# Kernel optimization log

Hardware: AMD Instinct MI355X
Metric: run time of the kernel (lower is better)

Reference implementation:

```python
import jax, jax.numpy as jnp
import numpy as np

B, T, C, NH = 2, 2048, 1024, 16
HD = C // NH  # 64


def _ln(x, g, b, eps=1e-5):
    m = x.mean(-1, keepdims=True)
    v = ((x - m) ** 2).mean(-1, keepdims=True)
    return (x - m) / jnp.sqrt(v + eps) * g + b


def _ff(x, w1, b1, w2, b2):
    # Linear -> exact (erf) GELU -> Linear; dropout=0 (identity)
    return jax.nn.gelu(x @ w1 + b1, approximate=False) @ w2 + b2


def setup_inputs() -> dict:
    key = jax.random.key(0)
    ks = jax.random.split(key, 16)
    s = 0.02
    f32 = jnp.float32
    return {
        "x": jax.random.normal(ks[0], (B, T, C), f32),
        # SelfAttn qkv projection (torch Linear stored transposed: (in, out))
        "w_attn": jax.random.normal(ks[1], (C, 3 * C), f32) * s,
        "b_attn": jnp.zeros((3 * C,), f32),
        # SelfAttn's internal FeedForward
        "wa1": jax.random.normal(ks[2], (C, 4 * C), f32) * s,
        "ba1": jnp.zeros((4 * C,), f32),
        "wa2": jax.random.normal(ks[3], (4 * C, C), f32) * s,
        "ba2": jnp.zeros((C,), f32),
        # Block ln1
        "g1": jnp.ones((C,), f32),
        "be1": jnp.zeros((C,), f32),
        # Block FeedForward
        "wf1": jax.random.normal(ks[4], (C, 4 * C), f32) * s,
        "bf1": jnp.zeros((4 * C,), f32),
        "wf2": jax.random.normal(ks[5], (4 * C, C), f32) * s,
        "bf2": jnp.zeros((C,), f32),
        # Block ln2
        "g2": jnp.ones((C,), f32),
        "be2": jnp.zeros((C,), f32),
    }


def reference(x, w_attn, b_attn, wa1, ba1, wa2, ba2, g1, be1,
              wf1, bf1, wf2, bf2, g2, be2):
    Bx, Tx, Cx = x.shape
    qkv = x @ w_attn + b_attn  # (B, T, 3C)
    # NOTE: original splits as K, Q, V (in that order)
    K, Q, V = jnp.split(qkv, 3, axis=-1)

    def heads(t):  # (B, T, C) -> (B, NH, T, HD)
        return t.reshape(Bx, Tx, NH, HD).transpose(0, 2, 1, 3)

    Q, K, V = heads(Q), heads(K), heads(V)
    att = jnp.einsum('bhqd,bhkd->bhqk', Q, K) / np.float32(np.sqrt(HD))
    mask = jnp.tril(jnp.ones((Tx, Tx), bool))  # causal
    att = jnp.where(mask, att, -jnp.inf)
    att = jax.nn.softmax(att, axis=-1)
    y = jnp.einsum('bhqk,bhkd->bhqd', att, V)
    y = y.transpose(0, 2, 1, 3).reshape(Bx, Tx, Cx)
    # SelfAttn applies its own FeedForward (no output projection)
    y = _ff(y, wa1, ba1, wa2, ba2)
    # Block: post-sublayer LayerNorm, additive residuals
    x = x + _ln(y, g1, be1)
    x = x + _ln(_ff(x, wf1, bf1, wf2, bf2), g2, be2)
    return x
```

## Files before the change

kernel.cpp:

```cpp
#include <hip/hip_runtime.h>
#include <hip/hip_bf16.h>
#include <math.h>

#define Bz 2
#define Tz 2048
#define Cz 1024
#define NHz 16
#define HDz 64
#define Mz (Bz*Tz)

typedef unsigned short u16;
typedef __attribute__((ext_vector_type(8))) short bf16x8;
typedef __attribute__((ext_vector_type(4))) float f32x4;

__device__ __forceinline__ float bf2f(u16 u){
  union { unsigned int i; float f; } v; v.i = ((unsigned int)u) << 16; return v.f;
}
__device__ __forceinline__ u16 f2bf(float f){
  union { float f; unsigned int i; } v; v.f = f;
  return (u16)((v.i + 0x7fffu + ((v.i >> 16) & 1u)) >> 16);
}
__device__ __forceinline__ unsigned pack_bf_trunc(float a, float b){
  union { float f; unsigned u; } ua, ub; ua.f = a; ub.f = b;
  return (ua.u >> 16) | (ub.u & 0xffff0000u);
}
__device__ __forceinline__ float gelu_fast(float x){
  float x3 = x * x * x;
  float z2 = 1.5957691216057308f * (x + 0.044715f * x3);
  float e  = __expf(z2);
  float t  = 1.f - 2.f / (e + 1.f);
  return 0.5f * x * (1.f + t);
}

__device__ __forceinline__ void glds16(const void* g, void* l){
  __builtin_amdgcn_global_load_lds(
      (const __attribute__((address_space(1))) void*)g,
      (__attribute__((address_space(3))) void*)l, 16, 0, 0);
}

__device__ __forceinline__ void pbar(){
  asm volatile("" ::: "memory");
  __builtin_amdgcn_s_barrier();
  asm volatile("" ::: "memory");
}
#define VMCNT(n) asm volatile("s_waitcnt vmcnt(" #n ")" ::: "memory")

__global__ __launch_bounds__(256) void cast4_kernel(const float* __restrict__ in,
                                                    u16* __restrict__ out, int n4){
  int i = blockIdx.x * 256 + threadIdx.x;
  if (i < n4) {
    float4 v = ((const float4*)in)[i];
    u16 t[4] = { f2bf(v.x), f2bf(v.y), f2bf(v.z), f2bf(v.w) };
    *(uint2*)&out[(size_t)i * 4] = *(const uint2*)t;
  }
}

__global__ __launch_bounds__(256) void transpose5_kernel(
    const float* __restrict__ s0, const float* __restrict__ s1,
    const float* __restrict__ s2, const float* __restrict__ s3,
    const float* __restrict__ s4,
    u16* __restrict__ d0, u16* __restrict__ d1, u16* __restrict__ d2,
    u16* __restrict__ d3, u16* __restrict__ d4){
  __shared__ float tile[32][33];
  const int t = blockIdx.x;
  const float* src; u16* dst; int K, N, local;
  if (t < 3072)       { src = s0; dst = d0; K = 1024; N = 3072; local = t; }
  else if (t < 7168)  { src = s1; dst = d1; K = 1024; N = 4096; local = t - 3072; }
  else if (t < 11264) { src = s2; dst = d2; K = 4096; N = 1024; local = t - 7168; }
  else if (t < 15360) { src = s3; dst = d3; K = 1024; N = 4096; local = t - 11264; }
  else                { src = s4; dst = d4; K = 4096; N = 1024; local = t - 15360; }
  const int NT = N >> 5;
  const int kb = (local / NT) * 32, nb = (local % NT) * 32;
  const int tx = threadIdx.x & 31, ty = threadIdx.x >> 5;
  #pragma unroll
  for (int r = ty; r < 32; r += 8)
    tile[r][tx] = src[(size_t)(kb + r) * N + nb + tx];
  __syncthreads();
  #pragma unroll
  for (int r = ty; r < 32; r += 8)
    dst[(size_t)(nb + r) * K + kb + tx] = f2bf(tile[tx][r]);
}

template<int ACT>
__global__ __launch_bounds__(512, 2) void gemm256_kernel(const u16* __restrict__ A,
                                                         const u16* __restrict__ Bt,
                                                         const float* __restrict__ bias,
                                                         u16* __restrict__ ob,
                                                         int N, int lda, int klen){
  __shared__ __align__(16) u16 As[2][256 * 64];
  __shared__ __align__(16) u16 Bs[2][256 * 64];
  const int tid  = threadIdx.x;
  const int lane = tid & 63;
  const int wave = tid >> 6;
  const int cc = lane & 15, quad = lane >> 4;
  const int wm = (wave >> 2) * 128;
  const int wn = (wave & 3) * 64;

  int flat = blockIdx.x + gridDim.x * blockIdx.y;
  const int nwg = gridDim.x * gridDim.y;
  flat = (flat & 7) * (nwg >> 3) + (flat >> 3);
  const int m0 = (flat & 15) * 256;
  const int n0 = (flat >> 4) * 256;

  const u16* Ak  = A  + (size_t)blockIdx.z * klen;
  const u16* Btk = Bt + (size_t)blockIdx.z * klen;

  int srow[2], scol[2];
  #pragma unroll
  for (int rnd = 0; rnd < 2; ++rnd) {
    const int ci = tid + rnd * 512;
    const int r = ci >> 3, cg = ci & 7;
    srow[rnd] = r;
    scol[rnd] = (cg ^ (r & 7)) * 8;
  }
  int colsw[2];
  #pragma unroll
  for (int s = 0; s < 2; ++s)
    colsw[s] = (s * 32 + quad * 8) ^ ((cc & 7) << 3);

  const auto stA = [&](int h, int t) {
    u16* dst = &As[t & 1][h * 8192];
    const u16* src = Ak + (size_t)(m0 + h * 128) * lda + t * 64;
    #pragma unroll
    for (int rnd = 0; rnd < 2; ++rnd)
      glds16(src + (size_t)srow[rnd] * lda + scol[rnd], dst + (tid + rnd * 512) * 8);
  };
  const auto stB = [&](int h, int t) {
    u16* dst = &Bs[t & 1][h * 8192];
    const u16* src = Btk + (size_t)(n0 + h * 128) * lda + t * 64;
    #pragma unroll
    for (int rnd = 0; rnd < 2; ++rnd)
      glds16(src + (size_t)srow[rnd] * lda + scol[rnd], dst + (tid + rnd * 512) * 8);
  };

  bf16x8 af[4][2];
  bf16x8 bfr[2][2][2];
  f32x4 acc[2][2][4][2] = {};

  const auto rdA = [&](int qa, int bsel) {
    #pragma unroll
    for (int f = 0; f < 4; ++f)
      #pragma unroll
      for (int s = 0; s < 2; ++s)
        af[f][s] = *(const bf16x8*)&As[bsel][(wm + qa * 64 + f * 16 + cc) * 64 + colsw[s]];
  };
  const auto rdB = [&](int qb, int bsel) {
    #pragma unroll
    for (int f = 0; f < 2; ++f)
      #pragma unroll
      for (int s = 0; s < 2; ++s)
        bfr[qb][f][s] = *(const bf16x8*)&Bs[bsel][(wn + qb * 32 + f * 16 + cc) * 64 + colsw[s]];
  };
  const auto mf16 = [&](int qa, int qb) {
    __builtin_amdgcn_s_setprio(1);
    #pragma unroll
    for (int s = 0; s < 2; ++s)
      #pragma unroll
      for (int am = 0; am < 4; ++am)
        #pragma unroll
        for (int bn = 0; bn < 2; ++bn)
          acc[qa][qb][am][bn] = __builtin_amdgcn_mfma_f32_16x16x32_bf16(
              af[am][s], bfr[qb][bn][s], acc[qa][qb][am][bn], 0, 0, 0);
    __builtin_amdgcn_s_setprio(0);
  };

  stA(0, 0); stB(0, 0); stA(1, 0); stB(1, 0);
  stA(0, 1); stB(1, 1);
  VMCNT(4);
  pbar();

  const int nIter = klen >> 7;
  for (int i = 0; i < nIter; ++i) {
    const int t = 2 * i;
    const bool more = (i + 1 < nIter);
    rdA(0, 0); rdB(0, 0); stA(1, t + 1);
    pbar(); mf16(0, 0); pbar();
    rdB(1, 0); stB(0, t + 1);
    pbar(); mf16(0, 1); pbar();
    rdA(1, 0); if (more) stA(0, t + 2);
    pbar(); mf16(1, 1); pbar();
    if (more) stB(1, t + 2);
    pbar(); mf16(1, 0);
    if (more) { VMCNT(4); } else { VMCNT(0); }
    pbar();
    rdA(0, 1); rdB(0, 1); if (more) stA(1, t + 2);
    pbar(); mf16(0, 0); pbar();
    rdB(1, 1); if (more) stB(0, t + 2);
    pbar(); mf16(0, 1); pbar();
    rdA(1, 1); if (more) stA(0, t + 3);
    pbar(); mf16(1, 1); pbar();
    if (more) stB(1, t + 3);
    pbar(); mf16(1, 0);
    if (more) { VMCNT(4); }
    pbar();
  }

  u16* obz = ob + (size_t)blockIdx.z * ((size_t)Mz * N);
  const float* bp = (blockIdx.z == 0) ? bias : nullptr;
  #pragma unroll
  for (int qa = 0; qa < 2; ++qa)
    #pragma unroll
    for (int qb = 0; qb < 2; ++qb)
      #pragma unroll
      for (int bn = 0; bn < 2; ++bn) {
        const int col = n0 + wn + qb * 32 + bn * 16 + cc;
        const float bv = bp ? bp[col] : 0.f;
        #pragma unroll
        for (int am = 0; am < 4; ++am)
          #pragma unroll
          for (int r = 0; r < 4; ++r) {
            const int row = m0 + wm + qa * 64 + am * 16 + quad * 4 + r;
            float v = acc[qa][qb][am][bn][r] + bv;
            if (ACT == 1) v = gelu_fast(v);
            obz[(size_t)row * N + col] = f2bf(v);
          }
      }
}

__global__ __launch_bounds__(256) void vtrans_kernel(const u16* __restrict__ qkv,
                                                     u16* __restrict__ Vtb){
  __shared__ u16 Vl[64 * 72];
  const int tid = threadIdx.x;
  const int t0 = blockIdx.x * 64, h = blockIdx.y, b = blockIdx.z;
  const int bh = b * NHz + h;
  #pragma unroll
  for (int it = 0; it < 2; it++) {
    int c = tid + it * 256;
    int row = c >> 3, g = c & 7;
    *(uint4*)&Vl[row * 72 + g * 8] =
        *(const uint4*)(qkv + (size_t)(b * Tz + t0 + row) * (3 * Cz) + 2 * Cz + h * 64 + g * 8);
  }
  __syncthreads();
  #pragma unroll
  for (int it = 0; it < 2; it++) {
    int c = tid + it * 256;
    int d = c >> 3, tg = c & 7;
    u16 tmp[8];
    #pragma unroll
    for (int e = 0; e < 8; e++) tmp[e] = Vl[(tg * 8 + e) * 72 + d];
    *(uint4*)&Vtb[((size_t)bh * 64 + d) * Tz + t0 + tg * 8] = *(const uint4*)tmp;
  }
}

__global__ __launch_bounds__(256) void attn_kernel(const u16* __restrict__ qkv,
                                                   const u16* __restrict__ Vtb,
                                                   u16* __restrict__ y){
  __shared__ __align__(16) u16 KV[2][2][64 * 64];
  __shared__ __align__(16) u16 Ps[64 * 72];
  const int tid = threadIdx.x;
  const int lane = tid & 63, wave = tid >> 6;
  const int cc = lane & 15, quad = lane >> 4;
  const int h = blockIdx.y, b = blockIdx.z;
  const int bh = b * NHz + h;
  const size_t rowb = (size_t)b * Tz;
  const int wq0 = wave * 16;

  int foff[4][2];
  const int sw0 = (quad ^ (cc & 7)) * 8;
  const int sw1 = ((4 + quad) ^ (cc & 7)) * 8;
  #pragma unroll
  for (int t = 0; t < 4; ++t) {
    foff[t][0] = (t * 16 + cc) * 64 + sw0;
    foff[t][1] = (t * 16 + cc) * 64 + sw1;
  }
  const int pswb = (wq0 + cc) * 72 + quad * 4;
  const int psr0 = (wq0 + cc) * 72 + quad * 8;
  const int psr1 = (wq0 + cc) * 72 + 32 + quad * 8;

  auto stage = [&](int i, int bsel) {
    const int k0s = i * 64;
    #pragma unroll
    for (int it = 0; it < 2; ++it) {
      int ci = tid + it * 256;
      int row = ci >> 3, g = ci & 7;
      int gs = g ^ (row & 7);
      glds16(qkv + (rowb + k0s + row) * (3 * Cz) + h * 64 + gs * 8, &KV[bsel][0][ci * 8]);
      glds16(Vtb + ((size_t)bh * 64 + row) * Tz + k0s + gs * 8,     &KV[bsel][1][ci * 8]);
    }
  };

  for (int ph = 0; ph < 2; ++ph) {
    const int qt = ph ? (31 - (int)blockIdx.x) : (int)blockIdx.x;
    const int q0t = qt * 64 + wq0;
    const int nkt = qt + 1;
    const int wqmax = q0t + 15;

    bf16x8 qf[2];
    #pragma unroll
    for (int s = 0; s < 2; ++s)
      qf[s] = *(const bf16x8*)(qkv + (rowb + q0t + cc) * (3 * Cz)
                               + Cz + h * 64 + s * 32 + quad * 8);
    f32x4 acc[4] = {};
    float lp = 0.f;

    if (ph) __syncthreads();
    stage(0, 0);

    for (int i = 0; i < nkt; ++i) {
      __syncthreads();
      if (i + 1 < nkt) stage(i + 1, (i + 1) & 1);
      const int sel = i & 1;
      const u16* Kl = KV[sel][0];
      const u16* Vl = KV[sel][1];
      const int k0 = i * 64;
      if (k0 > wqmax) continue;

      bf16x8 kf[4][2];
      #pragma unroll
      for (int kt = 0; kt < 4; ++kt) {
        kf[kt][0] = *(const bf16x8*)&Kl[foff[kt][0]];
        kf[kt][1] = *(const bf16x8*)&Kl[foff[kt][1]];
      }
      const int qbase = q0t;
      #pragma unroll
      for (int kt = 0; kt < 4; ++kt) {
        const int kbase = k0 + kt * 16;
        uint2 pk;
        if (kbase > qbase + 15) {
          pk.x = 0u; pk.y = 0u;
        } else {
          f32x4 st = __builtin_amdgcn_mfma_f32_16x16x32_bf16(
              kf[kt][0], qf[0], (f32x4){0.f, 0.f, 0.f, 0.f}, 0, 0, 0);
          st = __builtin_amdgcn_mfma_f32_16x16x32_bf16(kf[kt][1], qf[1], st, 0, 0, 0);
          if (kbase + 15 > qbase) {
            const int kq = kbase + quad * 4, ql = qbase + cc;
            st[0] = (kq     <= ql) ? st[0] : -1e30f;
            st[1] = (kq + 1 <= ql) ? st[1] : -1e30f;
            st[2] = (kq + 2 <= ql) ? st[2] : -1e30f;
            st[3] = (kq + 3 <= ql) ? st[3] : -1e30f;
          }
          float p0 = __expf(fmaf(st[0], 0.125f, -16.f));
          float p1 = __expf(fmaf(st[1], 0.125f, -16.f));
          float p2 = __expf(fmaf(st[2], 0.125f, -16.f));
          float p3 = __expf(fmaf(st[3], 0.125f, -16.f));
          lp += (p0 + p1) + (p2 + p3);
          pk.x = pack_bf_trunc(p0, p1);
          pk.y = pack_bf_trunc(p2, p3);
        }
        *(uint2*)&Ps[pswb + kt * 16] = pk;
      }
      bf16x8 pf0 = *(const bf16x8*)&Ps[psr0];
      bf16x8 pf1 = *(const bf16x8*)&Ps[psr1];
      #pragma unroll
      for (int jd = 0; jd < 4; ++jd) {
        bf16x8 vf0 = *(const bf16x8*)&Vl[foff[jd][0]];
        bf16x8 vf1 = *(const bf16x8*)&Vl[foff[jd][1]];
        acc[jd] = __builtin_amdgcn_mfma_f32_16x16x32_bf16(pf0, vf0, acc[jd], 0, 0, 0);
        acc[jd] = __builtin_amdgcn_mfma_f32_16x16x32_bf16(pf1, vf1, acc[jd], 0, 0, 0);
      }
    }

    lp += __shfl_xor(lp, 16, 64);
    lp += __shfl_xor(lp, 32, 64);
    float inv[4];
    #pragma unroll
    for (int r = 0; r < 4; ++r) inv[r] = 1.f / __shfl(lp, quad * 4 + r, 64);
    #pragma unroll
    for (int jd = 0; jd < 4; ++jd)
      #pragma unroll
      for (int r = 0; r < 4; ++r) {
        int qrow = q0t + quad * 4 + r;
        y[(rowb + qrow) * Cz + h * 64 + jd * 16 + cc] = f2bf(acc[jd][r] * inv[r]);
      }
  }
}

__global__ __launch_bounds__(256) void ln_resid_kernel(const float* __restrict__ xf,
                                                       const u16* __restrict__ xb16,
                                                       const u16* __restrict__ yp,
                                                       const float* __restrict__ g,
                                                       const float* __restrict__ be,
                                                       float* __restrict__ outf,
                                                       u16* __restrict__ outb){
  const int row = blockIdx.x;
  const int c0 = threadIdx.x * 4;
  const size_t base = (size_t)row * Cz + c0;
  float4 v; v.x = 0.f; v.y = 0.f; v.z = 0.f; v.w = 0.f;
  #pragma unroll
  for (int p = 0; p < 4; ++p) {
    uint2 pp = *(const uint2*)(yp + (size_t)p * ((size_t)Mz * Cz) + base);
    v.x += bf2f((u16)(pp.x & 0xffff)); v.y += bf2f((u16)(pp.x >> 16));
    v.z += bf2f((u16)(pp.y & 0xffff)); v.w += bf2f((u16)(pp.y >> 16));
  }
  float s  = v.x + v.y + v.z + v.w;
  float s2 = v.x*v.x + v.y*v.y + v.z*v.z + v.w*v.w;
  #pragma unroll
  for (int off = 32; off > 0; off >>= 1) {
    s  += __shfl_down(s,  off);
    s2 += __shfl_down(s2, off);
  }
  __shared__ float ps[4], ps2[4];
  int wave = threadIdx.x >> 6, lane = threadIdx.x & 63;
  if (lane == 0) { ps[wave] = s; ps2[wave] = s2; }
  __syncthreads();
  s  = ps[0]  + ps[1]  + ps[2]  + ps[3];
  s2 = ps2[0] + ps2[1] + ps2[2] + ps2[3];
  const float mean = s * (1.f / Cz);
  const float var  = s2 * (1.f / Cz) - mean * mean;
  const float rstd = rsqrtf(var + 1e-5f);
  float4 xv;
  if (xf) {
    xv = *(const float4*)(xf + base);
  } else {
    uint2 px = *(const uint2*)(xb16 + base);
    xv.x = bf2f((u16)(px.x & 0xffff)); xv.y = bf2f((u16)(px.x >> 16));
    xv.z = bf2f((u16)(px.y & 0xffff)); xv.w = bf2f((u16)(px.y >> 16));
  }
  float4 gv = *(const float4*)(g + c0);
  float4 bv = *(const float4*)(be + c0);
  float4 ov;
  ov.x = xv.x + (v.x - mean) * rstd * gv.x + bv.x;
  ov.y = xv.y + (v.y - mean) * rstd * gv.y + bv.y;
  ov.z = xv.z + (v.z - mean) * rstd * gv.z + bv.z;
  ov.w = xv.w + (v.w - mean) * rstd * gv.w + bv.w;
  if (outf) *(float4*)(outf + base) = ov;
  if (outb) {
    u16 t[4] = { f2bf(ov.x), f2bf(ov.y), f2bf(ov.z), f2bf(ov.w) };
    *(ulonglong1*)&outb[base] = *(const ulonglong1*)t;
  }
}

extern "C" void kernel_launch(void* const* d_in, const int* in_sizes, int n_in,
                              void* d_out, int out_size, void* d_ws, size_t ws_size,
                              hipStream_t stream) {
  const float* x      = (const float*)d_in[0];
  const float* w_attn = (const float*)d_in[1];
  const float* b_attn = (const float*)d_in[2];
  const float* wa1    = (const float*)d_in[3];
  const float* ba1    = (const float*)d_in[4];
  const float* wa2    = (const float*)d_in[5];
  const float* ba2    = (const float*)d_in[6];
  const float* g1     = (const float*)d_in[7];
  const float* be1    = (const float*)d_in[8];
  const float* wf1    = (const float*)d_in[9];
  const float* bf1    = (const float*)d_in[10];
  const float* wf2    = (const float*)d_in[11];
  const float* bf2    = (const float*)d_in[12];
  const float* g2     = (const float*)d_in[13];
  const float* be2    = (const float*)d_in[14];
  float* out = (float*)d_out;

  char* ws = (char*)d_ws;
  size_t off = 0;
  auto alloc = [&](size_t bytes) { size_t o = off; off += (bytes + 255) & ~(size_t)255; return o; };
  u16* qkvb    = (u16*)(ws + alloc((size_t)Mz * 3 * Cz * 2));
  u16* ybuf    = (u16*)(ws + alloc((size_t)Mz * Cz * 2));
  u16* xb      = (u16*)(ws + alloc((size_t)Mz * Cz * 2));
  u16* wT_attn = (u16*)(ws + alloc((size_t)3 * Cz * Cz * 2));
  u16* wT_a1   = (u16*)(ws + alloc((size_t)4 * Cz * Cz * 2));
  u16* Vtb     = (u16*)(ws + alloc((size_t)Bz * NHz * HDz * Tz * 2));
  u16* wT_a2   = (u16*)(ws + alloc((size_t)4 * Cz * Cz * 2));
  u16* wT_f1   = (u16*)(ws + alloc((size_t)4 * Cz * Cz * 2));
  u16* wT_f2   = (u16*)(ws + alloc((size_t)4 * Cz * Cz * 2));
  u16* hbuf    = (u16*)(ws + alloc((size_t)Mz * 4 * Cz * 2));
  u16* pb      = (u16*)(ws + alloc((size_t)4 * Mz * Cz * 2));
  u16* x1b     = (u16*)(ws + alloc((size_t)Mz * Cz * 2));
  alloc(256);
  (void)ws_size; (void)in_sizes; (void)n_in; (void)out_size;

  cast4_kernel<<<(Mz * Cz / 4 + 255) / 256, 256, 0, stream>>>(x, xb, Mz * Cz / 4);
  transpose5_kernel<<<19456, 256, 0, stream>>>(w_attn, wa1, wa2, wf1, wf2,
                                               wT_attn, wT_a1, wT_a2, wT_f1, wT_f2);

  gemm256_kernel<0><<<dim3(16, 12, 1), 512, 0, stream>>>(xb, wT_attn, b_attn,
      qkvb, 3*Cz, Cz, Cz);

  vtrans_kernel<<<dim3(Tz/64, NHz, Bz), 256, 0, stream>>>(qkvb, Vtb);
  attn_kernel<<<dim3(16, NHz, Bz), 256, 0, stream>>>(qkvb, Vtb, ybuf);

  gemm256_kernel<1><<<dim3(16, 16, 1), 512, 0, stream>>>(ybuf, wT_a1, ba1,
      hbuf, 4*Cz, Cz, Cz);
  gemm256_kernel<0><<<dim3(16, 4, 4), 512, 0, stream>>>(hbuf, wT_a2, ba2,
      pb, Cz, 4*Cz, Cz);

  ln_resid_kernel<<<Mz, 256, 0, stream>>>(x, nullptr, pb, g1, be1,
                                          nullptr, x1b);

  gemm256_kernel<1><<<dim3(16, 16, 1), 512, 0, stream>>>(x1b, wT_f1, bf1,
      hbuf, 4*Cz, Cz, Cz);
  gemm256_kernel<0><<<dim3(16, 4, 4), 512, 0, stream>>>(hbuf, wT_f2, bf2,
      pb, Cz, 4*Cz, Cz);

  ln_resid_kernel<<<Mz, 256, 0, stream>>>(nullptr, x1b, pb, g2, be2,
                                          out, nullptr);
}
```

Measured before the change: 462.8 us.

## Stage GEMM epilogue through LDS, reorder loads, XCD-map attention blocks

The GEMM epilogue now writes bias+activation results into swizzled shared memory in four passes, then stores coalesced 16-byte rows to global memory instead of scattered 2-byte stores. K length becomes a template constant, and the prefetch order of A/B stages is shuffled. The attention grid is flattened to 512 blocks with an XCD-aware mapping so each chiplet's blocks share the same heads' K/V in L2. The epilogue adds extra barriers and reuses the As buffer after the main loop.

```diff
diff --git a/kernel.cpp b/kernel.cpp
--- a/kernel.cpp
+++ b/kernel.cpp
@@ -81,12 +81,12 @@
     dst[(size_t)(nb + r) * K + kb + tx] = f2bf(tile[tx][r]);
 }
 
-template<int ACT>
+template<int ACT, int KLEN>
 __global__ __launch_bounds__(512, 2) void gemm256_kernel(const u16* __restrict__ A,
                                                          const u16* __restrict__ Bt,
                                                          const float* __restrict__ bias,
                                                          u16* __restrict__ ob,
-                                                         int N, int lda, int klen){
+                                                         int N, int lda){
   __shared__ __align__(16) u16 As[2][256 * 64];
   __shared__ __align__(16) u16 Bs[2][256 * 64];
   const int tid  = threadIdx.x;
@@ -102,8 +102,8 @@
   const int m0 = (flat & 15) * 256;
   const int n0 = (flat >> 4) * 256;
 
-  const u16* Ak  = A  + (size_t)blockIdx.z * klen;
-  const u16* Btk = Bt + (size_t)blockIdx.z * klen;
+  const u16* Ak  = A  + (size_t)blockIdx.z * KLEN;
+  const u16* Btk = Bt + (size_t)blockIdx.z * KLEN;
 
   int srow[2], scol[2];
   #pragma unroll
@@ -164,30 +164,30 @@
     __builtin_amdgcn_s_setprio(0);
   };
 
-  stA(0, 0); stB(0, 0); stA(1, 0); stB(1, 0);
-  stA(0, 1); stB(1, 1);
+  stB(0, 0); stB(1, 0); stA(0, 0); stA(1, 0);
+  stB(0, 1); stB(1, 1);
   VMCNT(4);
   pbar();
 
-  const int nIter = klen >> 7;
+  constexpr int nIter = KLEN >> 7;
   for (int i = 0; i < nIter; ++i) {
     const int t = 2 * i;
     const bool more = (i + 1 < nIter);
-    rdA(0, 0); rdB(0, 0); stA(1, t + 1);
+    rdA(0, 0); rdB(0, 0); stA(0, t + 1);
     pbar(); mf16(0, 0); pbar();
-    rdB(1, 0); stB(0, t + 1);
+    rdB(1, 0); stA(1, t + 1);
     pbar(); mf16(0, 1); pbar();
-    rdA(1, 0); if (more) stA(0, t + 2);
+    rdA(1, 0); if (more) stB(0, t + 2);
     pbar(); mf16(1, 1); pbar();
     if (more) stB(1, t + 2);
     pbar(); mf16(1, 0);
     if (more) { VMCNT(4); } else { VMCNT(0); }
     pbar();
-    rdA(0, 1); rdB(0, 1); if (more) stA(1, t + 2);
+    rdA(0, 1); rdB(0, 1); if (more) stA(0, t + 2);
     pbar(); mf16(0, 0); pbar();
-    rdB(1, 1); if (more) stB(0, t + 2);
+    rdB(1, 1); if (more) stA(1, t + 2);
     pbar(); mf16(0, 1); pbar();
-    rdA(1, 1); if (more) stA(0, t + 3);
+    rdA(1, 1); if (more) stB(0, t + 3);
     pbar(); mf16(1, 1); pbar();
     if (more) stB(1, t + 3);
     pbar(); mf16(1, 0);
@@ -195,26 +195,42 @@
     pbar();
   }
 
+  u16* eb = (u16*)As;
   u16* obz = ob + (size_t)blockIdx.z * ((size_t)Mz * N);
   const float* bp = (blockIdx.z == 0) ? bias : nullptr;
   #pragma unroll
-  for (int qa = 0; qa < 2; ++qa)
-    #pragma unroll
-    for (int qb = 0; qb < 2; ++qb)
-      #pragma unroll
-      for (int bn = 0; bn < 2; ++bn) {
-        const int col = n0 + wn + qb * 32 + bn * 16 + cc;
-        const float bv = bp ? bp[col] : 0.f;
+  for (int pass = 0; pass < 4; ++pass) {
+    pbar();
+    if (wm == (pass >> 1) * 128) {
+      constexpr int dummy = 0; (void)dummy;
+      const int qaa = pass & 1;
+      #pragma unroll
+      for (int qb = 0; qb < 2; ++qb)
         #pragma unroll
-        for (int am = 0; am < 4; ++am)
+        for (int bn = 0; bn < 2; ++bn) {
+          const int col = wn + qb * 32 + bn * 16 + cc;
+          const float bv = bp ? bp[n0 + col] : 0.f;
           #pragma unroll
-          for (int r = 0; r < 4; ++r) {
-            const int row = m0 + wm + qa * 64 + am * 16 + quad * 4 + r;
-            float v = acc[qa][qb][am][bn][r] + bv;
-            if (ACT == 1) v = gelu_fast(v);
-            obz[(size_t)row * N + col] = f2bf(v);
-          }
-      }
+          for (int am = 0; am < 4; ++am)
+            #pragma unroll
+            for (int r = 0; r < 4; ++r) {
+              const int rl = am * 16 + quad * 4 + r;
+              float v = acc[qaa][qb][am][bn][r] + bv;
+              if (ACT == 1) v = gelu_fast(v);
+              eb[rl * 256 + (((col * 2) ^ ((rl & 7) << 4)) >> 1)] = f2bf(v);
+            }
+        }
+    }
+    pbar();
+    #pragma unroll
+    for (int c2 = 0; c2 < 4; ++c2) {
+      const int byteoff = (tid + c2 * 512) * 16;
+      const int rl = byteoff >> 9;
+      const int cb = byteoff & 511;
+      bf16x8 vv = *(const bf16x8*)((const char*)eb + rl * 512 + (cb ^ ((rl & 7) << 4)));
+      *(bf16x8*)((char*)obz + ((size_t)(m0 + pass * 64 + rl) * N + n0) * 2 + cb) = vv;
+    }
+  }
 }
 
 __global__ __launch_bounds__(256) void vtrans_kernel(const u16* __restrict__ qkv,
@@ -250,7 +266,11 @@
   const int tid = threadIdx.x;
   const int lane = tid & 63, wave = tid >> 6;
   const int cc = lane & 15, quad = lane >> 4;
-  const int h = blockIdx.y, b = blockIdx.z;
+  const int flat = blockIdx.x;
+  const int xcd = flat & 7, slot = flat >> 3;
+  const int bhg = xcd * 4 + (slot >> 4);
+  const int qtp = slot & 15;
+  const int h = bhg & 15, b = bhg >> 4;
   const int bh = b * NHz + h;
   const size_t rowb = (size_t)b * Tz;
   const int wq0 = wave * 16;
@@ -280,7 +300,7 @@
   };
 
   for (int ph = 0; ph < 2; ++ph) {
-    const int qt = ph ? (31 - (int)blockIdx.x) : (int)blockIdx.x;
+    const int qt = ph ? (31 - qtp) : qtp;
     const int q0t = qt * 64 + wq0;
     const int nkt = qt + 1;
     const int wqmax = q0t + 15;
@@ -462,24 +482,24 @@
   transpose5_kernel<<<19456, 256, 0, stream>>>(w_attn, wa1, wa2, wf1, wf2,
                                                wT_attn, wT_a1, wT_a2, wT_f1, wT_f2);
 
-  gemm256_kernel<0><<<dim3(16, 12, 1), 512, 0, stream>>>(xb, wT_attn, b_attn,
-      qkvb, 3*Cz, Cz, Cz);
+  gemm256_kernel<0, Cz><<<dim3(16, 12, 1), 512, 0, stream>>>(xb, wT_attn, b_attn,
+      qkvb, 3*Cz, Cz);
 
   vtrans_kernel<<<dim3(Tz/64, NHz, Bz), 256, 0, stream>>>(qkvb, Vtb);
-  attn_kernel<<<dim3(16, NHz, Bz), 256, 0, stream>>>(qkvb, Vtb, ybuf);
-
-  gemm256_kernel<1><<<dim3(16, 16, 1), 512, 0, stream>>>(ybuf, wT_a1, ba1,
-      hbuf, 4*Cz, Cz, Cz);
-  gemm256_kernel<0><<<dim3(16, 4, 4), 512, 0, stream>>>(hbuf, wT_a2, ba2,
-      pb, Cz, 4*Cz, Cz);
+  attn_kernel<<<dim3(512, 1, 1), 256, 0, stream>>>(qkvb, Vtb, ybuf);
+
+  gemm256_kernel<1, Cz><<<dim3(16, 16, 1), 512, 0, stream>>>(ybuf, wT_a1, ba1,
+      hbuf, 4*Cz, Cz);
+  gemm256_kernel<0, Cz><<<dim3(16, 4, 4), 512, 0, stream>>>(hbuf, wT_a2, ba2,
+      pb, Cz, 4*Cz);
 
   ln_resid_kernel<<<Mz, 256, 0, stream>>>(x, nullptr, pb, g1, be1,
                                           nullptr, x1b);
 
-  gemm256_kernel<1><<<dim3(16, 16, 1), 512, 0, stream>>>(x1b, wT_f1, bf1,
-      hbuf, 4*Cz, Cz, Cz);
-  gemm256_kernel<0><<<dim3(16, 4, 4), 512, 0, stream>>>(hbuf, wT_f2, bf2,
-      pb, Cz, 4*Cz, Cz);
+  gemm256_kernel<1, Cz><<<dim3(16, 16, 1), 512, 0, stream>>>(x1b, wT_f1, bf1,
+      hbuf, 4*Cz, Cz);
+  gemm256_kernel<0, Cz><<<dim3(16, 4, 4), 512, 0, stream>>>(hbuf, wT_f2, bf2,
+      pb, Cz, 4*Cz);
 
   ln_resid_kernel<<<Mz, 256, 0, stream>>>(nullptr, x1b, pb, g2, be2,
                                           out, nullptr);
```

Result: no change. 462.9 us (+0.0%).
